# Optimization experiments

Measured on AMD Instinct MI355X. Metric: run time of the kernel, lower is better.

Reference implementation:

```python
import jax, jax.numpy as jnp
import numpy as np

EMBED_DIM = 512
N_HEADS = 8
HEAD_DIM = EMBED_DIM // N_HEADS
N_BINS = 512
MAX_BIN = 256
SCALE = 1.0 / np.sqrt(HEAD_DIM)


def _l2norm(x):
    # manifold.project onto unit sphere along last dim
    n = jnp.sqrt(jnp.sum(x * x, axis=-1, keepdims=True))
    return x / jnp.maximum(n, 1e-12)


def setup_inputs() -> dict:
    rng = jax.random.key(0)
    ks = jax.random.split(rng, 13)
    B, N, D = 1, 2048, EMBED_DIM
    s = 1.0 / np.sqrt(D)
    cen = jax.random.normal(ks[12], (N_BINS, HEAD_DIM), dtype=jnp.float32)
    return {
        "query": jax.random.normal(ks[0], (B, N, D), dtype=jnp.float32),
        "key": jax.random.normal(ks[1], (B, N, D), dtype=jnp.float32),
        "value": jax.random.normal(ks[2], (B, N, D), dtype=jnp.float32),
        "Wq": jax.random.normal(ks[3], (D, D), dtype=jnp.float32) * s,
        "bq": jax.random.normal(ks[4], (D,), dtype=jnp.float32) * s,
        "Wk": jax.random.normal(ks[5], (D, D), dtype=jnp.float32) * s,
        "bk": jax.random.normal(ks[6], (D,), dtype=jnp.float32) * s,
        "Wv": jax.random.normal(ks[7], (D, D), dtype=jnp.float32) * s,
        "bv": jax.random.normal(ks[8], (D,), dtype=jnp.float32) * s,
        "Wo": jax.random.normal(ks[9], (D, D), dtype=jnp.float32) * s,
        "bo": jax.random.normal(ks[10], (D,), dtype=jnp.float32) * s,
        "centroids": _l2norm(cen),  # unit bin centroids of dim head_dim
    }


def reference(query, key, value, Wq, bq, Wk, bk, Wv, bv, Wo, bo, centroids):
    B, Nq, D = query.shape
    Nk = key.shape[1]
    H, hd = N_HEADS, HEAD_DIM

    def split(x):  # [B,N,D] -> [B,H,N,hd]
        return x.reshape(B, -1, H, hd).transpose(0, 2, 1, 3)

    q = split(query @ Wq.T + bq)
    k = split(key @ Wk.T + bk)
    v = split(value @ Wv.T + bv)

    # manifold.project (sphere): attention uses the projected q/k, raw v
    qn = _l2norm(q)
    kn = _l2norm(k)

    # DavisCache: nearest-centroid bin id  [B,H,N]
    qb = jnp.argmax(jnp.einsum('bhnd,cd->bhnc', qn, centroids), axis=-1).astype(jnp.int32)
    kb = jnp.argmax(jnp.einsum('bhnd,cd->bhnc', kn, centroids), axis=-1).astype(jnp.int32)

    # neighboring_bins(qb, radius=1) on a ring: kb in {qb-1, qb, qb+1} mod N_BINS
    diff = (qb[..., :, None] - kb[..., None, :]) % N_BINS  # [B,H,Nq,Nk]
    neigh = (diff <= 1) | (diff >= N_BINS - 1)

    # truncate to first MAX_BIN selected keys (index order), as in the loop
    rank = jnp.cumsum(neigh.astype(jnp.int32), axis=-1)  # inclusive count
    sel = neigh & (rank <= MAX_BIN)
    # fallback: empty neighbor set -> all keys, then truncated to first MAX_BIN
    fallback = (jnp.arange(Nk, dtype=jnp.int32) < MAX_BIN)
    mask = jnp.where(neigh.any(axis=-1, keepdims=True), sel, fallback)

    scores = jnp.einsum('bhqd,bhkd->bhqk', qn, kn) * jnp.float32(SCALE)
    scores = jnp.where(mask, scores, jnp.float32(-1e30))
    attn = jax.nn.softmax(scores, axis=-1)  # dropout=0.0 (eval)
    out = jnp.einsum('bhqk,bhkd->bhqd', attn, v)

    out = out.transpose(0, 2, 1, 3).reshape(B, Nq, D)
    return out @ Wo.T + bo
```

## Files before the change

### kernel.cpp

```cpp
#include <hip/hip_runtime.h>
#include <hip/hip_bf16.h>

#define NTOK 2048
#define EMBED 512
#define NHEADS 8
#define HD 64
#define NBINS 512
#define MAXSEL 256

typedef unsigned short u16;
typedef unsigned int u32;

__device__ __forceinline__ float lof(u32 u){ return __uint_as_float(u << 16); }
__device__ __forceinline__ float hif(u32 u){ return __uint_as_float(u & 0xffff0000u); }
__device__ __forceinline__ float bf2f(u16 u){ return __uint_as_float(((u32)u) << 16); }
__device__ __forceinline__ u16 f2b(float f){
    __hip_bfloat16 h = __float2bfloat16(f);
    return *(u16*)&h;
}
__device__ __forceinline__ u32 pack2(float lo, float hi){
    return (u32)f2b(lo) | ((u32)f2b(hi) << 16);
}
__device__ __forceinline__ void fma8(const float* x, u32 ux, u32 uy, u32 uz, u32 uw, float& a){
    a += x[0]*lof(ux) + x[1]*hif(ux) + x[2]*lof(uy) + x[3]*hif(uy)
       + x[4]*lof(uz) + x[5]*hif(uz) + x[6]*lof(uw) + x[7]*hif(uw);
}

__device__ __forceinline__ u32 sniffp(const void* p){
    const u16* s = (const u16*)p;
    float m = 0.f;
    #pragma unroll
    for (int k=0; k<64; k++) m = fmaxf(m, fabsf(bf2f(s[2*k])));
    return (m > 100.f) ? 1u : 0u;
}

__global__ __launch_bounds__(256) void projqkv_kernel(
    const void* __restrict__ Xq, const void* __restrict__ Xk, const void* __restrict__ Xv,
    const void* __restrict__ Wq, const void* __restrict__ bq,
    const void* __restrict__ Wk, const void* __restrict__ bk,
    const void* __restrict__ Wv, const void* __restrict__ bv,
    const void* __restrict__ cen,
    void* __restrict__ outQ,
    u16* __restrict__ Kb, u16* __restrict__ Vb,
    u16* __restrict__ qbin, u16* __restrict__ kbin)
{
    int which = blockIdx.y;
    const void *X, *W, *Bb;
    if (which==0){ X=Xq; W=Wq; Bb=bq; }
    else if (which==1){ X=Xk; W=Wk; Bb=bk; }
    else { X=Xv; W=Wv; Bb=bv; }
    u32 fx = sniffp(X), fw = sniffp(W), fb = sniffp(Bb);
    int r0 = blockIdx.x * 8;
    int t = threadIdx.x;

    __shared__ __align__(16) float ubuf[4608];
    __shared__ __align__(16) float ps[64*65];
    __shared__ float nrm2[64][4];
    __shared__ float invn[64];
    __shared__ float bvl[64][8];
    __shared__ int   bil[64][8];

    float* xstage = ps;
    for (int i=t; i<1024; i+=256){
        int row = i>>7, c4 = i&127;
        float4 v;
        if (!fx){
            const u32* xp = (const u32*)((const u16*)X + (size_t)(r0+row)*EMBED);
            u32 a = xp[c4*2], b = xp[c4*2+1];
            v = make_float4(lof(a), hif(a), lof(b), hif(b));
        } else {
            v = ((const float4*)((const float*)X + (size_t)(r0+row)*EMBED))[c4];
        }
        *(float4*)(xstage + row*516 + c4*4) = v;
    }

    float acc2[8][2];
    #pragma unroll
    for (int r=0;r<8;r++){ acc2[r][0]=0.f; acc2[r][1]=0.f; }

    float4 pf[4];
    #pragma unroll
    for (int it=0; it<4; it++){
        int j = t + it*256, o = j>>1, half = j&1;
        if (!fw){
            const u32* wp2 = (const u32*)((const u16*)W + (size_t)o*EMBED + half*4);
            pf[it] = make_float4(lof(wp2[0]), hif(wp2[0]), lof(wp2[1]), hif(wp2[1]));
        } else {
            pf[it] = *(const float4*)((const float*)W + (size_t)o*EMBED + half*4);
        }
    }
    for (int k0=0; k0<512; k0+=8){
        __syncthreads();
        #pragma unroll
        for (int it=0; it<4; it++){
            int j = t + it*256, o = j>>1, kb = (j&1)*4;
            ubuf[o*9+kb+0]=pf[it].x; ubuf[o*9+kb+1]=pf[it].y;
            ubuf[o*9+kb+2]=pf[it].z; ubuf[o*9+kb+3]=pf[it].w;
        }
        if (k0+8 < 512){
            int kn = k0+8;
            #pragma unroll
            for (int it=0; it<4; it++){
                int j = t + it*256, o = j>>1, half = j&1;
                if (!fw){
                    const u32* wp2 = (const u32*)((const u16*)W + (size_t)o*EMBED + kn + half*4);
                    pf[it] = make_float4(lof(wp2[0]), hif(wp2[0]), lof(wp2[1]), hif(wp2[1]));
                } else {
                    pf[it] = *(const float4*)((const float*)W + (size_t)o*EMBED + kn + half*4);
                }
            }
        }
        __syncthreads();
        float w0[8], w1[8];
        #pragma unroll
        for (int kk=0;kk<8;kk++){
            w0[kk] = ubuf[t*9+kk];
            w1[kk] = ubuf[(t+256)*9+kk];
        }
        #pragma unroll
        for (int r=0;r<8;r++){
            const float* x = xstage + r*516 + k0;
            float4 x0 = *(const float4*)(x);
            float4 x1 = *(const float4*)(x+4);
            acc2[r][0] += x0.x*w0[0]+x0.y*w0[1]+x0.z*w0[2]+x0.w*w0[3]
                        + x1.x*w0[4]+x1.y*w0[5]+x1.z*w0[6]+x1.w*w0[7];
            acc2[r][1] += x0.x*w1[0]+x0.y*w1[1]+x0.z*w1[2]+x0.w*w1[3]
                        + x1.x*w1[4]+x1.y*w1[5]+x1.z*w1[6]+x1.w*w1[7];
        }
    }
    __syncthreads();
    {
        float b0 = fb ? ((const float*)Bb)[t]     : bf2f(((const u16*)Bb)[t]);
        float b1 = fb ? ((const float*)Bb)[t+256] : bf2f(((const u16*)Bb)[t+256]);
        int h0 = t>>6, c0 = t&63, h1 = (t+256)>>6, c1 = (t+256)&63;
        #pragma unroll
        for (int r=0;r<8;r++){
            ps[(r*8+h0)*65 + c0] = acc2[r][0]+b0;
            ps[(r*8+h1)*65 + c1] = acc2[r][1]+b1;
        }
    }
    __syncthreads();

    if (which == 2){
        int hr = t>>2, q4 = t&3;
        int row = hr>>3, head = hr&7;
        const float* src = ps + hr*65 + q4*16;
        u16* dst = Vb + (size_t)(r0+row)*EMBED + head*64 + q4*16;
        #pragma unroll
        for (int j8=0;j8<2;j8++){
            uint4 v;
            v.x = pack2(src[j8*8+0],src[j8*8+1]); v.y = pack2(src[j8*8+2],src[j8*8+3]);
            v.z = pack2(src[j8*8+4],src[j8*8+5]); v.w = pack2(src[j8*8+6],src[j8*8+7]);
            ((uint4*)dst)[j8] = v;
        }
        return;
    }

    u32 fc = sniffp(cen);
    int rg = t>>3, cg = t&7;
    float best[2] = {-3.4e38f,-3.4e38f};
    int   bidx[2] = {0,0};
    float cpre[16];
    #pragma unroll
    for (int it=0; it<16; it++){
        int e = t + it*256, j = e>>6, k = e&63;
        cpre[it] = fc ? ((const float*)cen)[(size_t)j*HD + k]
                      : bf2f(((const u16*)cen)[(size_t)j*HD + k]);
    }
    for (int tt=0; tt<8; tt++){
        __syncthreads();
        #pragma unroll
        for (int it=0; it<16; it++){
            int e = t + it*256, j = e>>6, k = e&63;
            ubuf[k*68 + j] = cpre[it];
        }
        if (tt < 7){
            #pragma unroll
            for (int it=0; it<16; it++){
                int e = t + it*256, j = e>>6, k = e&63;
                int gj = (tt+1)*64 + j;
                cpre[it] = fc ? ((const float*)cen)[(size_t)gj*HD + k]
                              : bf2f(((const u16*)cen)[(size_t)gj*HD + k]);
            }
        }
        __syncthreads();
        float acc[2][8];
        #pragma unroll
        for (int j=0;j<2;j++)
            #pragma unroll
            for (int c=0;c<8;c++) acc[j][c]=0.f;
        const float* pr0 = ps + (2*rg)*65;
        const float* pr1 = pr0 + 65;
        for (int k=0;k<64;k++){
            float a0 = pr0[k], a1 = pr1[k];
            const float4* cp = (const float4*)(ubuf + k*68 + cg*8);
            float4 c0 = cp[0], c1 = cp[1];
            acc[0][0]+=a0*c0.x; acc[0][1]+=a0*c0.y; acc[0][2]+=a0*c0.z; acc[0][3]+=a0*c0.w;
            acc[0][4]+=a0*c1.x; acc[0][5]+=a0*c1.y; acc[0][6]+=a0*c1.z; acc[0][7]+=a0*c1.w;
            acc[1][0]+=a1*c0.x; acc[1][1]+=a1*c0.y; acc[1][2]+=a1*c0.z; acc[1][3]+=a1*c0.w;
            acc[1][4]+=a1*c1.x; acc[1][5]+=a1*c1.y; acc[1][6]+=a1*c1.z; acc[1][7]+=a1*c1.w;
        }
        #pragma unroll
        for (int j=0;j<2;j++){
            #pragma unroll
            for (int c=0;c<8;c++){
                int gi = tt*64 + cg*8 + c;
                if (acc[j][c] > best[j]){ best[j]=acc[j][c]; bidx[j]=gi; }
            }
        }
    }
    bvl[2*rg  ][cg]=best[0]; bil[2*rg  ][cg]=bidx[0];
    bvl[2*rg+1][cg]=best[1]; bil[2*rg+1][cg]=bidx[1];
    {
        int hr = t>>2, q4 = t&3;
        const float* src = ps + hr*65 + q4*16;
        float ss=0.f;
        #pragma unroll
        for (int d=0;d<16;d++) ss += src[d]*src[d];
        nrm2[hr][q4]=ss;
    }
    __syncthreads();
    if (t < 64){
        int hr = t;
        invn[hr] = 1.f / fmaxf(sqrtf(nrm2[hr][0]+nrm2[hr][1]+nrm2[hr][2]+nrm2[hr][3]), 1e-12f);
        float bv = bvl[hr][0]; int bi = bil[hr][0];
        #pragma unroll
        for (int g=1; g<8; g++){
            float ov = bvl[hr][g]; int oi = bil[hr][g];
            if (ov > bv || (ov == bv && oi < bi)){ bv = ov; bi = oi; }
        }
        u16* bins = (which==0) ? qbin : kbin;
        int token = r0 + (hr>>3), head = hr&7;
        bins[head*NTOK + token] = (u16)bi;
    }
    __syncthreads();
    {
        int hr = t>>2, q4 = t&3;
        float inv = invn[hr];
        const float* src = ps + hr*65 + q4*16;
        int row = hr>>3, head = hr&7;
        size_t off = (size_t)(r0+row)*EMBED + head*64 + q4*16;
        if (which == 1){
            u16* dst = Kb + off;
            #pragma unroll
            for (int j8=0;j8<2;j8++){
                uint4 v;
                v.x = pack2(src[j8*8+0]*inv, src[j8*8+1]*inv);
                v.y = pack2(src[j8*8+2]*inv, src[j8*8+3]*inv);
                v.z = pack2(src[j8*8+4]*inv, src[j8*8+5]*inv);
                v.w = pack2(src[j8*8+6]*inv, src[j8*8+7]*inv);
                ((uint4*)dst)[j8] = v;
            }
        } else if (!fx){
            u16* dst = (u16*)outQ + off;
            #pragma unroll
            for (int j8=0;j8<2;j8++){
                uint4 v;
                v.x = pack2(src[j8*8+0]*inv, src[j8*8+1]*inv);
                v.y = pack2(src[j8*8+2]*inv, src[j8*8+3]*inv);
                v.z = pack2(src[j8*8+4]*inv, src[j8*8+5]*inv);
                v.w = pack2(src[j8*8+6]*inv, src[j8*8+7]*inv);
                ((uint4*)dst)[j8] = v;
            }
        } else {
            float* dst = (float*)outQ + off;
            #pragma unroll
            for (int j4=0;j4<4;j4++){
                float4 v = make_float4(src[j4*4+0]*inv, src[j4*4+1]*inv,
                                       src[j4*4+2]*inv, src[j4*4+3]*inv);
                ((float4*)dst)[j4] = v;
            }
        }
    }
}

__global__ __launch_bounds__(256) void attn_kernel(
    const void* __restrict__ query,
    const u16* __restrict__ Kb, const u16* __restrict__ Vb,
    const u16* __restrict__ qbin, const u16* __restrict__ kbin,
    void* __restrict__ out)
{
    u32 fq = sniffp(query);
    int q = blockIdx.x, t = threadIdx.x;
    int wave = t>>6, lane = t&63;
    __shared__ float qs[512];
    __shared__ float sc[4][256];
    __shared__ u16   sel[4][256];

    if (!fq){
        u32 u = ((const u32*)out)[(size_t)q*256 + t];
        qs[2*t] = lof(u); qs[2*t+1] = hif(u);
    } else {
        float2 f = ((const float2*)out)[(size_t)q*256 + t];
        qs[2*t] = f.x; qs[2*t+1] = f.y;
    }
    __syncthreads();

    for (int hh=0; hh<2; hh++){
        int h = wave*2 + hh;
        int myqb = qbin[h*NTOK + q];
        const uint4* kbp = (const uint4*)(kbin + h*NTOK + lane*32);
        u32 fl = 0;
        #pragma unroll
        for (int w4=0; w4<4; w4++){
            uint4 kw = kbp[w4];
            u32 arr[4] = {kw.x, kw.y, kw.z, kw.w};
            #pragma unroll
            for (int e=0;e<4;e++){
                int b0 = (int)(arr[e] & 0xffff), b1 = (int)(arr[e] >> 16);
                int d0 = (myqb - b0) & (NBINS-1), d1 = (myqb - b1) & (NBINS-1);
                if (d0 <= 1 || d0 >= NBINS-1) fl |= 1u << (w4*8 + e*2);
                if (d1 <= 1 || d1 >= NBINS-1) fl |= 1u << (w4*8 + e*2 + 1);
            }
        }
        int cnt = __popc(fl);
        int sum = cnt;
        #pragma unroll
        for (int off=1; off<64; off<<=1){
            int v = __shfl_up(sum, off, 64);
            if (lane >= off) sum += v;
        }
        int total = __shfl(sum, 63, 64);
        int r = sum - cnt;
        if (total){
            u32 f2 = fl;
            while (f2){
                int j = __ffs(f2) - 1; f2 &= f2 - 1;
                if (r < MAXSEL) sel[wave][r] = (u16)(lane*32 + j);
                r++;
            }
        } else {
            #pragma unroll
            for (int kq=0;kq<4;kq++) sel[wave][lane*4+kq] = (u16)(lane*4+kq);
        }
        int L = total ? min(total, MAXSEL) : MAXSEL;
        __syncthreads();
        const float* qh = qs + h*64;
        float mloc = -3.4e38f;
        for (int jj=lane; jj<L; jj+=64){
            int kkey = sel[wave][jj];
            const uint4* kr = (const uint4*)(Kb + (size_t)kkey*EMBED + h*64);
            float acc = 0.f;
            #pragma unroll
            for (int p=0;p<8;p++){ uint4 u = kr[p]; fma8(qh+p*8, u.x,u.y,u.z,u.w, acc); }
            float s = acc * 0.125f;
            sc[wave][jj] = s;
            mloc = fmaxf(mloc, s);
        }
        #pragma unroll
        for (int off=32; off; off>>=1) mloc = fmaxf(mloc, __shfl_xor(mloc, off, 64));
        float ssum = 0.f;
        for (int jj=lane; jj<L; jj+=64){
            float e = __expf(sc[wave][jj] - mloc);
            sc[wave][jj] = e; ssum += e;
        }
        #pragma unroll
        for (int off=32; off; off>>=1) ssum += __shfl_xor(ssum, off, 64);
        float inv = 1.f / fmaxf(ssum, 1e-37f);
        __syncthreads();
        float acc = 0.f;
        for (int j=0; j<L; j++){
            int kkey = sel[wave][j];
            acc += sc[wave][j] * bf2f(Vb[(size_t)kkey*EMBED + h*64 + lane]);
        }
        float o = acc * inv;
        if (!fq) ((u16*)out)[(size_t)q*EMBED + h*64 + lane] = f2b(o);
        else     ((float*)out)[(size_t)q*EMBED + h*64 + lane] = o;
        __syncthreads();
    }
}

__global__ __launch_bounds__(256) void oproj_kernel(
    void* __restrict__ out, const void* __restrict__ Wo, const void* __restrict__ bo)
{
    u32 fq = sniffp(out);
    u32 fw = sniffp(Wo), fb = sniffp(bo);
    int r0 = blockIdx.x * 4;
    int t = threadIdx.x;
    __shared__ __align__(16) float wsl[512*9];
    __shared__ __align__(16) float xst[4*516];

    for (int i=t; i<512; i+=256){
        int row = i>>7, c4 = i&127;
        float4 v;
        if (!fq){
            const u32* xp = (const u32*)((const u16*)out + (size_t)(r0+row)*EMBED);
            u32 a = xp[c4*2], b = xp[c4*2+1];
            v = make_float4(lof(a), hif(a), lof(b), hif(b));
        } else {
            v = ((const float4*)((const float*)out + (size_t)(r0+row)*EMBED))[c4];
        }
        *(float4*)(xst + row*516 + c4*4) = v;
    }

    float acc2[4][2];
    #pragma unroll
    for (int r=0;r<4;r++){ acc2[r][0]=0.f; acc2[r][1]=0.f; }

    float4 pf[4];
    #pragma unroll
    for (int it=0; it<4; it++){
        int j = t + it*256, o = j>>1, half = j&1;
        if (!fw){
            const u32* wp2 = (const u32*)((const u16*)Wo + (size_t)o*EMBED + half*4);
            pf[it] = make_float4(lof(wp2[0]), hif(wp2[0]), lof(wp2[1]), hif(wp2[1]));
        } else {
            pf[it] = *(const float4*)((const float*)Wo + (size_t)o*EMBED + half*4);
        }
    }
    for (int k0=0; k0<512; k0+=8){
        __syncthreads();
        #pragma unroll
        for (int it=0; it<4; it++){
            int j = t + it*256, o = j>>1, kb = (j&1)*4;
            wsl[o*9+kb+0]=pf[it].x; wsl[o*9+kb+1]=pf[it].y;
            wsl[o*9+kb+2]=pf[it].z; wsl[o*9+kb+3]=pf[it].w;
        }
        if (k0+8 < 512){
            int kn = k0+8;
            #pragma unroll
            for (int it=0; it<4; it++){
                int j = t + it*256, o = j>>1, half = j&1;
                if (!fw){
                    const u32* wp2 = (const u32*)((const u16*)Wo + (size_t)o*EMBED + kn + half*4);
                    pf[it] = make_float4(lof(wp2[0]), hif(wp2[0]), lof(wp2[1]), hif(wp2[1]));
                } else {
                    pf[it] = *(const float4*)((const float*)Wo + (size_t)o*EMBED + kn + half*4);
                }
            }
        }
        __syncthreads();
        float w0[8], w1[8];
        #pragma unroll
        for (int kk=0;kk<8;kk++){
            w0[kk] = wsl[t*9+kk];
            w1[kk] = wsl[(t+256)*9+kk];
        }
        #pragma unroll
        for (int r=0;r<4;r++){
            const float* x = xst + r*516 + k0;
            float4 x0 = *(const float4*)(x);
            float4 x1 = *(const float4*)(x+4);
            acc2[r][0] += x0.x*w0[0]+x0.y*w0[1]+x0.z*w0[2]+x0.w*w0[3]
                        + x1.x*w0[4]+x1.y*w0[5]+x1.z*w0[6]+x1.w*w0[7];
            acc2[r][1] += x0.x*w1[0]+x0.y*w1[1]+x0.z*w1[2]+x0.w*w1[3]
                        + x1.x*w1[4]+x1.y*w1[5]+x1.z*w1[6]+x1.w*w1[7];
        }
    }
    float b0 = fb ? ((const float*)bo)[t]     : bf2f(((const u16*)bo)[t]);
    float b1 = fb ? ((const float*)bo)[t+256] : bf2f(((const u16*)bo)[t+256]);
    if (!fq){
        u16* o = (u16*)out;
        #pragma unroll
        for (int r=0;r<4;r++){
            o[(size_t)(r0+r)*EMBED + t]       = f2b(acc2[r][0]+b0);
            o[(size_t)(r0+r)*EMBED + t + 256] = f2b(acc2[r][1]+b1);
        }
    } else {
        float* o = (float*)out;
        #pragma unroll
        for (int r=0;r<4;r++){
            o[(size_t)(r0+r)*EMBED + t]       = acc2[r][0]+b0;
            o[(size_t)(r0+r)*EMBED + t + 256] = acc2[r][1]+b1;
        }
    }
}

extern "C" void kernel_launch(void* const* d_in, const int* in_sizes, int n_in,
                              void* d_out, int out_size, void* d_ws, size_t ws_size,
                              hipStream_t stream)
{
    const void* query = d_in[0];
    const void* key   = d_in[1];
    const void* value = d_in[2];
    const void* Wq = d_in[3];
    const void* bq = d_in[4];
    const void* Wk = d_in[5];
    const void* bk = d_in[6];
    const void* Wv = d_in[7];
    const void* bv = d_in[8];
    const void* Wo = d_in[9];
    const void* bo = d_in[10];
    const void* cen = d_in[11];

    char* ws = (char*)d_ws;
    u16* qbin = (u16*)ws;
    u16* kbin = (u16*)(ws + 32768);
    u16* Kb   = (u16*)(ws + 65536);
    u16* Vb   = (u16*)(ws + 65536 + (size_t)2*1024*1024);

    projqkv_kernel<<<dim3(256,3), 256, 0, stream>>>(query,key,value,Wq,bq,Wk,bk,Wv,bv,cen,
                                                    d_out,Kb,Vb,qbin,kbin);
    attn_kernel<<<2048, 256, 0, stream>>>(query,Kb,Vb,qbin,kbin,d_out);
    oproj_kernel<<<512, 256, 0, stream>>>(d_out,Wo,bo);
}
```

Before: 319.1 us.

## Double block size to 512 threads with split-K reduction and per-head waves

```diff
diff --git a/kernel.cpp b/kernel.cpp
--- a/kernel.cpp
+++ b/kernel.cpp
@@ -34,7 +34,7 @@
     return (m > 100.f) ? 1u : 0u;
 }
 
-__global__ __launch_bounds__(256) void projqkv_kernel(
+__global__ __launch_bounds__(512) void projqkv_kernel(
     const void* __restrict__ Xq, const void* __restrict__ Xk, const void* __restrict__ Xv,
     const void* __restrict__ Wq, const void* __restrict__ bq,
     const void* __restrict__ Wk, const void* __restrict__ bk,
@@ -52,16 +52,14 @@
     u32 fx = sniffp(X), fw = sniffp(W), fb = sniffp(Bb);
     int r0 = blockIdx.x * 8;
     int t = threadIdx.x;
-
-    __shared__ __align__(16) float ubuf[4608];
+    int ht = t & 255;
+    int hb = t >> 8;
+
+    __shared__ __align__(16) float wsl[512*17];
     __shared__ __align__(16) float ps[64*65];
-    __shared__ float nrm2[64][4];
-    __shared__ float invn[64];
-    __shared__ float bvl[64][8];
-    __shared__ int   bil[64][8];
-
     float* xstage = ps;
-    for (int i=t; i<1024; i+=256){
+
+    for (int i=t; i<1024; i+=512){
         int row = i>>7, c4 = i&127;
         float4 v;
         if (!fx){
@@ -79,47 +77,56 @@
     for (int r=0;r<8;r++){ acc2[r][0]=0.f; acc2[r][1]=0.f; }
 
     float4 pf[4];
-    #pragma unroll
-    for (int it=0; it<4; it++){
-        int j = t + it*256, o = j>>1, half = j&1;
+    {
+        int o = t;
         if (!fw){
-            const u32* wp2 = (const u32*)((const u16*)W + (size_t)o*EMBED + half*4);
-            pf[it] = make_float4(lof(wp2[0]), hif(wp2[0]), lof(wp2[1]), hif(wp2[1]));
+            const u32* lo = (const u32*)((const u16*)W + (size_t)o*EMBED);
+            const u32* hi = (const u32*)((const u16*)W + (size_t)o*EMBED + 256);
+            pf[0] = make_float4(lof(lo[0]),hif(lo[0]),lof(lo[1]),hif(lo[1]));
+            pf[1] = make_float4(lof(lo[2]),hif(lo[2]),lof(lo[3]),hif(lo[3]));
+            pf[2] = make_float4(lof(hi[0]),hif(hi[0]),lof(hi[1]),hif(hi[1]));
+            pf[3] = make_float4(lof(hi[2]),hif(hi[2]),lof(hi[3]),hif(hi[3]));
         } else {
-            pf[it] = *(const float4*)((const float*)W + (size_t)o*EMBED + half*4);
-        }
-    }
-    for (int k0=0; k0<512; k0+=8){
+            const float4* lo = (const float4*)((const float*)W + (size_t)o*EMBED);
+            const float4* hi = (const float4*)((const float*)W + (size_t)o*EMBED + 256);
+            pf[0]=lo[0]; pf[1]=lo[1]; pf[2]=hi[0]; pf[3]=hi[1];
+        }
+    }
+    for (int s=0; s<32; s++){
         __syncthreads();
-        #pragma unroll
-        for (int it=0; it<4; it++){
-            int j = t + it*256, o = j>>1, kb = (j&1)*4;
-            ubuf[o*9+kb+0]=pf[it].x; ubuf[o*9+kb+1]=pf[it].y;
-            ubuf[o*9+kb+2]=pf[it].z; ubuf[o*9+kb+3]=pf[it].w;
-        }
-        if (k0+8 < 512){
-            int kn = k0+8;
-            #pragma unroll
-            for (int it=0; it<4; it++){
-                int j = t + it*256, o = j>>1, half = j&1;
-                if (!fw){
-                    const u32* wp2 = (const u32*)((const u16*)W + (size_t)o*EMBED + kn + half*4);
-                    pf[it] = make_float4(lof(wp2[0]), hif(wp2[0]), lof(wp2[1]), hif(wp2[1]));
-                } else {
-                    pf[it] = *(const float4*)((const float*)W + (size_t)o*EMBED + kn + half*4);
-                }
+        {
+            float* wr = wsl + t*17;
+            wr[0]=pf[0].x; wr[1]=pf[0].y; wr[2]=pf[0].z; wr[3]=pf[0].w;
+            wr[4]=pf[1].x; wr[5]=pf[1].y; wr[6]=pf[1].z; wr[7]=pf[1].w;
+            wr[8]=pf[2].x; wr[9]=pf[2].y; wr[10]=pf[2].z; wr[11]=pf[2].w;
+            wr[12]=pf[3].x; wr[13]=pf[3].y; wr[14]=pf[3].z; wr[15]=pf[3].w;
+        }
+        if (s+1 < 32){
+            int o = t, klo = (s+1)*8, khi = 256 + (s+1)*8;
+            if (!fw){
+                const u32* lo = (const u32*)((const u16*)W + (size_t)o*EMBED + klo);
+                const u32* hi = (const u32*)((const u16*)W + (size_t)o*EMBED + khi);
+                pf[0] = make_float4(lof(lo[0]),hif(lo[0]),lof(lo[1]),hif(lo[1]));
+                pf[1] = make_float4(lof(lo[2]),hif(lo[2]),lof(lo[3]),hif(lo[3]));
+                pf[2] = make_float4(lof(hi[0]),hif(hi[0]),lof(hi[1]),hif(hi[1]));
+                pf[3] = make_float4(lof(hi[2]),hif(hi[2]),lof(hi[3]),hif(hi[3]));
+            } else {
+                const float4* lo = (const float4*)((const float*)W + (size_t)o*EMBED + klo);
+                const float4* hi = (const float4*)((const float*)W + (size_t)o*EMBED + khi);
+                pf[0]=lo[0]; pf[1]=lo[1]; pf[2]=hi[0]; pf[3]=hi[1];
             }
         }
         __syncthreads();
+        int coff = hb*8, kg = hb*256 + s*8;
         float w0[8], w1[8];
         #pragma unroll
         for (int kk=0;kk<8;kk++){
-            w0[kk] = ubuf[t*9+kk];
-            w1[kk] = ubuf[(t+256)*9+kk];
+            w0[kk] = wsl[ht*17 + coff + kk];
+            w1[kk] = wsl[(ht+256)*17 + coff + kk];
         }
         #pragma unroll
         for (int r=0;r<8;r++){
-            const float* x = xstage + r*516 + k0;
+            const float* x = xstage + r*516 + kg;
             float4 x0 = *(const float4*)(x);
             float4 x1 = *(const float4*)(x+4);
             acc2[r][0] += x0.x*w0[0]+x0.y*w0[1]+x0.z*w0[2]+x0.w*w0[3]
@@ -129,104 +136,104 @@
         }
     }
     __syncthreads();
-    {
-        float b0 = fb ? ((const float*)Bb)[t]     : bf2f(((const u16*)Bb)[t]);
-        float b1 = fb ? ((const float*)Bb)[t+256] : bf2f(((const u16*)Bb)[t+256]);
-        int h0 = t>>6, c0 = t&63, h1 = (t+256)>>6, c1 = (t+256)&63;
+    if (hb == 1){
+        float* red = wsl + ht*17;
+        #pragma unroll
+        for (int r=0;r<8;r++){ red[r*2]=acc2[r][0]; red[r*2+1]=acc2[r][1]; }
+    }
+    __syncthreads();
+    if (hb == 0){
+        const float* red = wsl + ht*17;
+        float b0 = fb ? ((const float*)Bb)[ht]     : bf2f(((const u16*)Bb)[ht]);
+        float b1 = fb ? ((const float*)Bb)[ht+256] : bf2f(((const u16*)Bb)[ht+256]);
+        int h0 = ht>>6, c0 = ht&63, h1 = (ht+256)>>6, c1 = (ht+256)&63;
         #pragma unroll
         for (int r=0;r<8;r++){
-            ps[(r*8+h0)*65 + c0] = acc2[r][0]+b0;
-            ps[(r*8+h1)*65 + c1] = acc2[r][1]+b1;
+            ps[(r*8+h0)*65 + c0] = acc2[r][0]+red[r*2]+b0;
+            ps[(r*8+h1)*65 + c1] = acc2[r][1]+red[r*2+1]+b1;
         }
     }
     __syncthreads();
 
     if (which == 2){
-        int hr = t>>2, q4 = t&3;
+        int hr = t>>3, seg = t&7;
         int row = hr>>3, head = hr&7;
-        const float* src = ps + hr*65 + q4*16;
-        u16* dst = Vb + (size_t)(r0+row)*EMBED + head*64 + q4*16;
-        #pragma unroll
-        for (int j8=0;j8<2;j8++){
-            uint4 v;
-            v.x = pack2(src[j8*8+0],src[j8*8+1]); v.y = pack2(src[j8*8+2],src[j8*8+3]);
-            v.z = pack2(src[j8*8+4],src[j8*8+5]); v.w = pack2(src[j8*8+6],src[j8*8+7]);
-            ((uint4*)dst)[j8] = v;
-        }
+        const float* src = ps + hr*65 + seg*8;
+        uint4 v;
+        v.x = pack2(src[0],src[1]); v.y = pack2(src[2],src[3]);
+        v.z = pack2(src[4],src[5]); v.w = pack2(src[6],src[7]);
+        *(uint4*)(Vb + (size_t)(r0+row)*EMBED + head*64 + seg*8) = v;
         return;
     }
 
     u32 fc = sniffp(cen);
     int rg = t>>3, cg = t&7;
-    float best[2] = {-3.4e38f,-3.4e38f};
-    int   bidx[2] = {0,0};
-    float cpre[16];
-    #pragma unroll
-    for (int it=0; it<16; it++){
-        int e = t + it*256, j = e>>6, k = e&63;
+    float best = -3.4e38f; int bidx = 0;
+    float cpre[8];
+    #pragma unroll
+    for (int it=0; it<8; it++){
+        int e = t + it*512, j = e>>6, k = e&63;
         cpre[it] = fc ? ((const float*)cen)[(size_t)j*HD + k]
                       : bf2f(((const u16*)cen)[(size_t)j*HD + k]);
     }
     for (int tt=0; tt<8; tt++){
         __syncthreads();
         #pragma unroll
-        for (int it=0; it<16; it++){
-            int e = t + it*256, j = e>>6, k = e&63;
-            ubuf[k*68 + j] = cpre[it];
+        for (int it=0; it<8; it++){
+            int e = t + it*512, j = e>>6, k = e&63;
+            wsl[k*68 + j] = cpre[it];
         }
         if (tt < 7){
             #pragma unroll
-            for (int it=0; it<16; it++){
-                int e = t + it*256, j = e>>6, k = e&63;
+            for (int it=0; it<8; it++){
+                int e = t + it*512, j = e>>6, k = e&63;
                 int gj = (tt+1)*64 + j;
                 cpre[it] = fc ? ((const float*)cen)[(size_t)gj*HD + k]
                               : bf2f(((const u16*)cen)[(size_t)gj*HD + k]);
             }
         }
         __syncthreads();
-        float acc[2][8];
-        #pragma unroll
-        for (int j=0;j<2;j++)
-            #pragma unroll
-            for (int c=0;c<8;c++) acc[j][c]=0.f;
-        const float* pr0 = ps + (2*rg)*65;
-        const float* pr1 = pr0 + 65;
+        float acc[8];
+        #pragma unroll
+        for (int c=0;c<8;c++) acc[c]=0.f;
+        const float* pr = ps + rg*65;
         for (int k=0;k<64;k++){
-            float a0 = pr0[k], a1 = pr1[k];
-            const float4* cp = (const float4*)(ubuf + k*68 + cg*8);
+            float a0 = pr[k];
+            const float4* cp = (const float4*)(wsl + k*68 + cg*8);
             float4 c0 = cp[0], c1 = cp[1];
-            acc[0][0]+=a0*c0.x; acc[0][1]+=a0*c0.y; acc[0][2]+=a0*c0.z; acc[0][3]+=a0*c0.w;
-            acc[0][4]+=a0*c1.x; acc[0][5]+=a0*c1.y; acc[0][6]+=a0*c1.z; acc[0][7]+=a0*c1.w;
-            acc[1][0]+=a1*c0.x; acc[1][1]+=a1*c0.y; acc[1][2]+=a1*c0.z; acc[1][3]+=a1*c0.w;
-            acc[1][4]+=a1*c1.x; acc[1][5]+=a1*c1.y; acc[1][6]+=a1*c1.z; acc[1][7]+=a1*c1.w;
-        }
-        #pragma unroll
-        for (int j=0;j<2;j++){
-            #pragma unroll
-            for (int c=0;c<8;c++){
-                int gi = tt*64 + cg*8 + c;
-                if (acc[j][c] > best[j]){ best[j]=acc[j][c]; bidx[j]=gi; }
-            }
-        }
-    }
-    bvl[2*rg  ][cg]=best[0]; bil[2*rg  ][cg]=bidx[0];
-    bvl[2*rg+1][cg]=best[1]; bil[2*rg+1][cg]=bidx[1];
+            acc[0]+=a0*c0.x; acc[1]+=a0*c0.y; acc[2]+=a0*c0.z; acc[3]+=a0*c0.w;
+            acc[4]+=a0*c1.x; acc[5]+=a0*c1.y; acc[6]+=a0*c1.z; acc[7]+=a0*c1.w;
+        }
+        #pragma unroll
+        for (int c=0;c<8;c++){
+            int gi = tt*64 + cg*8 + c;
+            if (acc[c] > best){ best=acc[c]; bidx=gi; }
+        }
+    }
+    __syncthreads();
+    float* bvlf = wsl;
+    int*   bilf = (int*)(wsl + 512);
+    float* nrmf = wsl + 1024;
+    float* invf = wsl + 1536;
+    bvlf[rg*8+cg] = best; bilf[rg*8+cg] = bidx;
     {
-        int hr = t>>2, q4 = t&3;
-        const float* src = ps + hr*65 + q4*16;
+        const float* src = ps + rg*65 + cg*8;
         float ss=0.f;
         #pragma unroll
-        for (int d=0;d<16;d++) ss += src[d]*src[d];
-        nrm2[hr][q4]=ss;
+        for (int d=0;d<8;d++) ss += src[d]*src[d];
+        nrmf[rg*8+cg]=ss;
     }
     __syncthreads();
     if (t < 64){
         int hr = t;
-        invn[hr] = 1.f / fmaxf(sqrtf(nrm2[hr][0]+nrm2[hr][1]+nrm2[hr][2]+nrm2[hr][3]), 1e-12f);
-        float bv = bvl[hr][0]; int bi = bil[hr][0];
+        float s2 = 0.f;
+        #pragma unroll
+        for (int p=0;p<8;p++) s2 += nrmf[hr*8+p];
+        invf[hr] = 1.f / fmaxf(sqrtf(s2), 1e-12f);
+        float bv = bvlf[hr*8]; int bi = bilf[hr*8];
         #pragma unroll
         for (int g=1; g<8; g++){
-            float ov = bvl[hr][g]; int oi = bil[hr][g];
+            float ov = bvlf[hr*8+g]; int oi = bilf[hr*8+g];
             if (ov > bv || (ov == bv && oi < bi)){ bv = ov; bi = oi; }
         }
         u16* bins = (which==0) ? qbin : kbin;
@@ -235,152 +242,130 @@
     }
     __syncthreads();
     {
-        int hr = t>>2, q4 = t&3;
-        float inv = invn[hr];
-        const float* src = ps + hr*65 + q4*16;
+        int hr = t>>3, seg = t&7;
+        float inv = invf[hr];
+        const float* src = ps + hr*65 + seg*8;
         int row = hr>>3, head = hr&7;
-        size_t off = (size_t)(r0+row)*EMBED + head*64 + q4*16;
+        size_t off = (size_t)(r0+row)*EMBED + head*64 + seg*8;
         if (which == 1){
-            u16* dst = Kb + off;
-            #pragma unroll
-            for (int j8=0;j8<2;j8++){
-                uint4 v;
-                v.x = pack2(src[j8*8+0]*inv, src[j8*8+1]*inv);
-                v.y = pack2(src[j8*8+2]*inv, src[j8*8+3]*inv);
-                v.z = pack2(src[j8*8+4]*inv, src[j8*8+5]*inv);
-                v.w = pack2(src[j8*8+6]*inv, src[j8*8+7]*inv);
-                ((uint4*)dst)[j8] = v;
-            }
+            uint4 v;
+            v.x = pack2(src[0]*inv, src[1]*inv); v.y = pack2(src[2]*inv, src[3]*inv);
+            v.z = pack2(src[4]*inv, src[5]*inv); v.w = pack2(src[6]*inv, src[7]*inv);
+            *(uint4*)(Kb + off) = v;
         } else if (!fx){
-            u16* dst = (u16*)outQ + off;
-            #pragma unroll
-            for (int j8=0;j8<2;j8++){
-                uint4 v;
-                v.x = pack2(src[j8*8+0]*inv, src[j8*8+1]*inv);
-                v.y = pack2(src[j8*8+2]*inv, src[j8*8+3]*inv);
-                v.z = pack2(src[j8*8+4]*inv, src[j8*8+5]*inv);
-                v.w = pack2(src[j8*8+6]*inv, src[j8*8+7]*inv);
-                ((uint4*)dst)[j8] = v;
-            }
+            uint4 v;
+            v.x = pack2(src[0]*inv, src[1]*inv); v.y = pack2(src[2]*inv, src[3]*inv);
+            v.z = pack2(src[4]*inv, src[5]*inv); v.w = pack2(src[6]*inv, src[7]*inv);
+            *(uint4*)((u16*)outQ + off) = v;
         } else {
             float* dst = (float*)outQ + off;
-            #pragma unroll
-            for (int j4=0;j4<4;j4++){
-                float4 v = make_float4(src[j4*4+0]*inv, src[j4*4+1]*inv,
-                                       src[j4*4+2]*inv, src[j4*4+3]*inv);
-                ((float4*)dst)[j4] = v;
-            }
-        }
-    }
-}
-
-__global__ __launch_bounds__(256) void attn_kernel(
+            ((float4*)dst)[0] = make_float4(src[0]*inv,src[1]*inv,src[2]*inv,src[3]*inv);
+            ((float4*)dst)[1] = make_float4(src[4]*inv,src[5]*inv,src[6]*inv,src[7]*inv);
+        }
+    }
+}
+
+__global__ __launch_bounds__(512) void attn_kernel(
     const void* __restrict__ query,
     const u16* __restrict__ Kb, const u16* __restrict__ Vb,
     const u16* __restrict__ qbin, const u16* __restrict__ kbin,
     void* __restrict__ out)
 {
     u32 fq = sniffp(query);
-    int q = blockIdx.x, t = threadIdx.x;
-    int wave = t>>6, lane = t&63;
-    __shared__ float qs[512];
-    __shared__ float sc[4][256];
-    __shared__ u16   sel[4][256];
-
-    if (!fq){
-        u32 u = ((const u32*)out)[(size_t)q*256 + t];
-        qs[2*t] = lof(u); qs[2*t+1] = hif(u);
+    int q = blockIdx.x;
+    int h = threadIdx.x >> 6;
+    int lane = threadIdx.x & 63;
+    __shared__ float qsh[8][64];
+    __shared__ float sc[8][256];
+    __shared__ u16   sel[8][256];
+
+    {
+        float qv;
+        if (!fq) qv = bf2f(((const u16*)out)[(size_t)q*EMBED + h*64 + lane]);
+        else     qv = ((const float*)out)[(size_t)q*EMBED + h*64 + lane];
+        qsh[h][lane] = qv;
+    }
+    int myqb = qbin[h*NTOK + q];
+    const uint4* kbp = (const uint4*)(kbin + h*NTOK + lane*32);
+    u32 fl = 0;
+    #pragma unroll
+    for (int w4=0; w4<4; w4++){
+        uint4 kw = kbp[w4];
+        u32 arr[4] = {kw.x, kw.y, kw.z, kw.w};
+        #pragma unroll
+        for (int e=0;e<4;e++){
+            int b0 = (int)(arr[e] & 0xffff), b1 = (int)(arr[e] >> 16);
+            int d0 = (myqb - b0) & (NBINS-1), d1 = (myqb - b1) & (NBINS-1);
+            if (d0 <= 1 || d0 >= NBINS-1) fl |= 1u << (w4*8 + e*2);
+            if (d1 <= 1 || d1 >= NBINS-1) fl |= 1u << (w4*8 + e*2 + 1);
+        }
+    }
+    int cnt = __popc(fl);
+    int sum = cnt;
+    #pragma unroll
+    for (int off=1; off<64; off<<=1){
+        int v = __shfl_up(sum, off, 64);
+        if (lane >= off) sum += v;
+    }
+    int total = __shfl(sum, 63, 64);
+    int r = sum - cnt;
+    if (total){
+        u32 f2 = fl;
+        while (f2){
+            int j = __ffs(f2) - 1; f2 &= f2 - 1;
+            if (r < MAXSEL) sel[h][r] = (u16)(lane*32 + j);
+            r++;
+        }
     } else {
-        float2 f = ((const float2*)out)[(size_t)q*256 + t];
-        qs[2*t] = f.x; qs[2*t+1] = f.y;
-    }
-    __syncthreads();
-
-    for (int hh=0; hh<2; hh++){
-        int h = wave*2 + hh;
-        int myqb = qbin[h*NTOK + q];
-        const uint4* kbp = (const uint4*)(kbin + h*NTOK + lane*32);
-        u32 fl = 0;
-        #pragma unroll
-        for (int w4=0; w4<4; w4++){
-            uint4 kw = kbp[w4];
-            u32 arr[4] = {kw.x, kw.y, kw.z, kw.w};
-            #pragma unroll
-            for (int e=0;e<4;e++){
-                int b0 = (int)(arr[e] & 0xffff), b1 = (int)(arr[e] >> 16);
-                int d0 = (myqb - b0) & (NBINS-1), d1 = (myqb - b1) & (NBINS-1);
-                if (d0 <= 1 || d0 >= NBINS-1) fl |= 1u << (w4*8 + e*2);
-                if (d1 <= 1 || d1 >= NBINS-1) fl |= 1u << (w4*8 + e*2 + 1);
-            }
-        }
-        int cnt = __popc(fl);
-        int sum = cnt;
-        #pragma unroll
-        for (int off=1; off<64; off<<=1){
-            int v = __shfl_up(sum, off, 64);
-            if (lane >= off) sum += v;
-        }
-        int total = __shfl(sum, 63, 64);
-        int r = sum - cnt;
-        if (total){
-            u32 f2 = fl;
-            while (f2){
-                int j = __ffs(f2) - 1; f2 &= f2 - 1;
-                if (r < MAXSEL) sel[wave][r] = (u16)(lane*32 + j);
-                r++;
-            }
-        } else {
-            #pragma unroll
-            for (int kq=0;kq<4;kq++) sel[wave][lane*4+kq] = (u16)(lane*4+kq);
-        }
-        int L = total ? min(total, MAXSEL) : MAXSEL;
-        __syncthreads();
-        const float* qh = qs + h*64;
-        float mloc = -3.4e38f;
-        for (int jj=lane; jj<L; jj+=64){
-            int kkey = sel[wave][jj];
-            const uint4* kr = (const uint4*)(Kb + (size_t)kkey*EMBED + h*64);
-            float acc = 0.f;
-            #pragma unroll
-            for (int p=0;p<8;p++){ uint4 u = kr[p]; fma8(qh+p*8, u.x,u.y,u.z,u.w, acc); }
-            float s = acc * 0.125f;
-            sc[wave][jj] = s;
-            mloc = fmaxf(mloc, s);
-        }
-        #pragma unroll
-        for (int off=32; off; off>>=1) mloc = fmaxf(mloc, __shfl_xor(mloc, off, 64));
-        float ssum = 0.f;
-        for (int jj=lane; jj<L; jj+=64){
-            float e = __expf(sc[wave][jj] - mloc);
-            sc[wave][jj] = e; ssum += e;
-        }
-        #pragma unroll
-        for (int off=32; off; off>>=1) ssum += __shfl_xor(ssum, off, 64);
-        float inv = 1.f / fmaxf(ssum, 1e-37f);
-        __syncthreads();
+        #pragma unroll
+        for (int kq=0;kq<4;kq++) sel[h][lane*4+kq] = (u16)(lane*4+kq);
+    }
+    int L = total ? min(total, MAXSEL) : MAXSEL;
+
+    const float* qh = qsh[h];
+    float mloc = -3.4e38f;
+    for (int jj=lane; jj<L; jj+=64){
+        int kkey = sel[h][jj];
+        const uint4* kr = (const uint4*)(Kb + (size_t)kkey*EMBED + h*64);
         float acc = 0.f;
-        for (int j=0; j<L; j++){
-            int kkey = sel[wave][j];
-            acc += sc[wave][j] * bf2f(Vb[(size_t)kkey*EMBED + h*64 + lane]);
-        }
-        float o = acc * inv;
-        if (!fq) ((u16*)out)[(size_t)q*EMBED + h*64 + lane] = f2b(o);
-        else     ((float*)out)[(size_t)q*EMBED + h*64 + lane] = o;
-        __syncthreads();
-    }
-}
-
-__global__ __launch_bounds__(256) void oproj_kernel(
+        #pragma unroll
+        for (int p=0;p<8;p++){ uint4 u = kr[p]; fma8(qh+p*8, u.x,u.y,u.z,u.w, acc); }
+        float s = acc * 0.125f;
+        sc[h][jj] = s;
+        mloc = fmaxf(mloc, s);
+    }
+    #pragma unroll
+    for (int off=32; off; off>>=1) mloc = fmaxf(mloc, __shfl_xor(mloc, off, 64));
+    float ssum = 0.f;
+    for (int jj=lane; jj<L; jj+=64){
+        float e = __expf(sc[h][jj] - mloc);
+        sc[h][jj] = e; ssum += e;
+    }
+    #pragma unroll
+    for (int off=32; off; off>>=1) ssum += __shfl_xor(ssum, off, 64);
+    float inv = 1.f / fmaxf(ssum, 1e-37f);
+    float acc = 0.f;
+    for (int j=0; j<L; j++){
+        int kkey = sel[h][j];
+        acc += sc[h][j] * bf2f(Vb[(size_t)kkey*EMBED + h*64 + lane]);
+    }
+    float o = acc * inv;
+    if (!fq) ((u16*)out)[(size_t)q*EMBED + h*64 + lane] = f2b(o);
+    else     ((float*)out)[(size_t)q*EMBED + h*64 + lane] = o;
+}
+
+__global__ __launch_bounds__(512) void oproj_kernel(
     void* __restrict__ out, const void* __restrict__ Wo, const void* __restrict__ bo)
 {
     u32 fq = sniffp(out);
     u32 fw = sniffp(Wo), fb = sniffp(bo);
     int r0 = blockIdx.x * 4;
     int t = threadIdx.x;
-    __shared__ __align__(16) float wsl[512*9];
+    int ht = t & 255, hb = t >> 8;
+    __shared__ __align__(16) float wsl[512*17];
     __shared__ __align__(16) float xst[4*516];
 
-    for (int i=t; i<512; i+=256){
+    for (int i=t; i<512; i+=512){
         int row = i>>7, c4 = i&127;
         float4 v;
         if (!fq){
@@ -398,47 +383,56 @@
     for (int r=0;r<4;r++){ acc2[r][0]=0.f; acc2[r][1]=0.f; }
 
     float4 pf[4];
-    #pragma unroll
-    for (int it=0; it<4; it++){
-        int j = t + it*256, o = j>>1, half = j&1;
+    {
+        int o = t;
         if (!fw){
-            const u32* wp2 = (const u32*)((const u16*)Wo + (size_t)o*EMBED + half*4);
-            pf[it] = make_float4(lof(wp2[0]), hif(wp2[0]), lof(wp2[1]), hif(wp2[1]));
+            const u32* lo = (const u32*)((const u16*)Wo + (size_t)o*EMBED);
+            const u32* hi = (const u32*)((const u16*)Wo + (size_t)o*EMBED + 256);
+            pf[0] = make_float4(lof(lo[0]),hif(lo[0]),lof(lo[1]),hif(lo[1]));
+            pf[1] = make_float4(lof(lo[2]),hif(lo[2]),lof(lo[3]),hif(lo[3]));
+            pf[2] = make_float4(lof(hi[0]),hif(hi[0]),lof(hi[1]),hif(hi[1]));
+            pf[3] = make_float4(lof(hi[2]),hif(hi[2]),lof(hi[3]),hif(hi[3]));
         } else {
-            pf[it] = *(const float4*)((const float*)Wo + (size_t)o*EMBED + half*4);
-        }
-    }
-    for (int k0=0; k0<512; k0+=8){
+            const float4* lo = (const float4*)((const float*)Wo + (size_t)o*EMBED);
+            const float4* hi = (const float4*)((const float*)Wo + (size_t)o*EMBED + 256);
+            pf[0]=lo[0]; pf[1]=lo[1]; pf[2]=hi[0]; pf[3]=hi[1];
+        }
+    }
+    for (int s=0; s<32; s++){
         __syncthreads();
-        #pragma unroll
-        for (int it=0; it<4; it++){
-            int j = t + it*256, o = j>>1, kb = (j&1)*4;
-            wsl[o*9+kb+0]=pf[it].x; wsl[o*9+kb+1]=pf[it].y;
-            wsl[o*9+kb+2]=pf[it].z; wsl[o*9+kb+3]=pf[it].w;
-        }
-        if (k0+8 < 512){
-            int kn = k0+8;
-            #pragma unroll
-            for (int it=0; it<4; it++){
-                int j = t + it*256, o = j>>1, half = j&1;
-                if (!fw){
-                    const u32* wp2 = (const u32*)((const u16*)Wo + (size_t)o*EMBED + kn + half*4);
-                    pf[it] = make_float4(lof(wp2[0]), hif(wp2[0]), lof(wp2[1]), hif(wp2[1]));
-                } else {
-                    pf[it] = *(const float4*)((const float*)Wo + (size_t)o*EMBED + kn + half*4);
-                }
+        {
+            float* wr = wsl + t*17;
+            wr[0]=pf[0].x; wr[1]=pf[0].y; wr[2]=pf[0].z; wr[3]=pf[0].w;
+            wr[4]=pf[1].x; wr[5]=pf[1].y; wr[6]=pf[1].z; wr[7]=pf[1].w;
+            wr[8]=pf[2].x; wr[9]=pf[2].y; wr[10]=pf[2].z; wr[11]=pf[2].w;
+            wr[12]=pf[3].x; wr[13]=pf[3].y; wr[14]=pf[3].z; wr[15]=pf[3].w;
+        }
+        if (s+1 < 32){
+            int o = t, klo = (s+1)*8, khi = 256 + (s+1)*8;
+            if (!fw){
+                const u32* lo = (const u32*)((const u16*)Wo + (size_t)o*EMBED + klo);
+                const u32* hi = (const u32*)((const u16*)Wo + (size_t)o*EMBED + khi);
+                pf[0] = make_float4(lof(lo[0]),hif(lo[0]),lof(lo[1]),hif(lo[1]));
+                pf[1] = make_float4(lof(lo[2]),hif(lo[2]),lof(lo[3]),hif(lo[3]));
+                pf[2] = make_float4(lof(hi[0]),hif(hi[0]),lof(hi[1]),hif(hi[1]));
+                pf[3] = make_float4(lof(hi[2]),hif(hi[2]),lof(hi[3]),hif(hi[3]));
+            } else {
+                const float4* lo = (const float4*)((const float*)Wo + (size_t)o*EMBED + klo);
+                const float4* hi = (const float4*)((const float*)Wo + (size_t)o*EMBED + khi);
+                pf[0]=lo[0]; pf[1]=lo[1]; pf[2]=hi[0]; pf[3]=hi[1];
             }
         }
         __syncthreads();
+        int coff = hb*8, kg = hb*256 + s*8;
         float w0[8], w1[8];
         #pragma unroll
         for (int kk=0;kk<8;kk++){
-            w0[kk] = wsl[t*9+kk];
-            w1[kk] = wsl[(t+256)*9+kk];
+            w0[kk] = wsl[ht*17 + coff + kk];
+            w1[kk] = wsl[(ht+256)*17 + coff + kk];
         }
         #pragma unroll
         for (int r=0;r<4;r++){
-            const float* x = xst + r*516 + k0;
+            const float* x = xst + r*516 + kg;
             float4 x0 = *(const float4*)(x);
             float4 x1 = *(const float4*)(x+4);
             acc2[r][0] += x0.x*w0[0]+x0.y*w0[1]+x0.z*w0[2]+x0.w*w0[3]
@@ -447,21 +441,31 @@
                         + x1.x*w1[4]+x1.y*w1[5]+x1.z*w1[6]+x1.w*w1[7];
         }
     }
-    float b0 = fb ? ((const float*)bo)[t]     : bf2f(((const u16*)bo)[t]);
-    float b1 = fb ? ((const float*)bo)[t+256] : bf2f(((const u16*)bo)[t+256]);
-    if (!fq){
-        u16* o = (u16*)out;
-        #pragma unroll
-        for (int r=0;r<4;r++){
-            o[(size_t)(r0+r)*EMBED + t]       = f2b(acc2[r][0]+b0);
-            o[(size_t)(r0+r)*EMBED + t + 256] = f2b(acc2[r][1]+b1);
-        }
-    } else {
-        float* o = (float*)out;
-        #pragma unroll
-        for (int r=0;r<4;r++){
-            o[(size_t)(r0+r)*EMBED + t]       = acc2[r][0]+b0;
-            o[(size_t)(r0+r)*EMBED + t + 256] = acc2[r][1]+b1;
+    __syncthreads();
+    if (hb == 1){
+        float* red = wsl + ht*9;
+        #pragma unroll
+        for (int r=0;r<4;r++){ red[r*2]=acc2[r][0]; red[r*2+1]=acc2[r][1]; }
+    }
+    __syncthreads();
+    if (hb == 0){
+        const float* red = wsl + ht*9;
+        float b0 = fb ? ((const float*)bo)[ht]     : bf2f(((const u16*)bo)[ht]);
+        float b1 = fb ? ((const float*)bo)[ht+256] : bf2f(((const u16*)bo)[ht+256]);
+        if (!fq){
+            u16* o = (u16*)out;
+            #pragma unroll
+            for (int r=0;r<4;r++){
+                o[(size_t)(r0+r)*EMBED + ht]       = f2b(acc2[r][0]+red[r*2]+b0);
+                o[(size_t)(r0+r)*EMBED + ht + 256] = f2b(acc2[r][1]+red[r*2+1]+b1);
+            }
+        } else {
+            float* o = (float*)out;
+            #pragma unroll
+            for (int r=0;r<4;r++){
+                o[(size_t)(r0+r)*EMBED + ht]       = acc2[r][0]+red[r*2]+b0;
+                o[(size_t)(r0+r)*EMBED + ht + 256] = acc2[r][1]+red[r*2+1]+b1;
+            }
         }
     }
 }
@@ -489,8 +493,8 @@
     u16* Kb   = (u16*)(ws + 65536);
     u16* Vb   = (u16*)(ws + 65536 + (size_t)2*1024*1024);
 
-    projqkv_kernel<<<dim3(256,3), 256, 0, stream>>>(query,key,value,Wq,bq,Wk,bk,Wv,bv,cen,
+    projqkv_kernel<<<dim3(256,3), 512, 0, stream>>>(query,key,value,Wq,bq,Wk,bk,Wv,bv,cen,
                                                     d_out,Kb,Vb,qbin,kbin);
-    attn_kernel<<<2048, 256, 0, stream>>>(query,Kb,Vb,qbin,kbin,d_out);
-    oproj_kernel<<<512, 256, 0, stream>>>(d_out,Wo,bo);
-}
+    attn_kernel<<<2048, 512, 0, stream>>>(query,Kb,Vb,qbin,kbin,d_out);
+    oproj_kernel<<<512, 512, 0, stream>>>(d_out,Wo,bo);
+}
```

Measured after the change: 372.3 us. 16.7% more time.
